# Optimization experiments

Hardware: AMD Instinct MI355X
Metric: run time of the kernel (lower is better)

The kernel has to match this reference:

```python
import jax, jax.numpy as jnp
import numpy as np

B, T, E, V, U = 4096, 80, 100, 10000, 1024


def setup_inputs() -> dict:
    key = jax.random.key(0)
    ks = jax.random.split(key, 8)
    def w(k, shape, fan_in):
        return jax.random.normal(k, shape, jnp.float32) * (1.0 / np.sqrt(fan_in))
    return {
        "inputs": jax.random.randint(ks[0], (B, T), 0, V, dtype=jnp.int32),
        "emb_table": w(ks[1], (V, E), E),
        "Wx0": w(ks[2], (E, U), E),
        "Wh0": w(ks[3], (U, U), U),
        "b0": jnp.zeros((U,), jnp.float32),
        "Wx1": w(ks[4], (U, U), U),
        "Wh1": w(ks[5], (U, U), U),
        "b1": jnp.zeros((U,), jnp.float32),
        "Wfc": w(ks[6], (U, 1), U),
        "bfc": jnp.zeros((1,), jnp.float32),
    }


def reference(inputs, emb_table, Wx0, Wh0, b0, Wx1, Wh1, b1, Wfc, bfc):
    # Embedding lookup: [B, T, E]
    x = emb_table[inputs]
    # Time-major for scan: [T, B, E]
    xs = jnp.swapaxes(x, 0, 1)
    h0_init = jnp.zeros((inputs.shape[0], Wh0.shape[0]), x.dtype)
    h1_init = jnp.zeros((inputs.shape[0], Wh1.shape[0]), x.dtype)

    def step(carry, xt):
        h0, h1 = carry
        # SimpleRNNCell: h' = tanh(x @ Wx + h @ Wh + b); output == new state
        h0 = jnp.tanh(xt @ Wx0 + h0 @ Wh0 + b0)
        h1 = jnp.tanh(h0 @ Wx1 + h1 @ Wh1 + b1)
        return (h0, h1), None

    (h0, h1), _ = jax.lax.scan(step, (h0_init, h1_init), xs)
    # Final dense + sigmoid on last layer-1 output
    prob = jax.nn.sigmoid(h1 @ Wfc + bfc)
    return prob
```

## Files before the change

kernel.cpp:

```cpp
#include <hip/hip_runtime.h>
#include <stdint.h>

#define B_ 4096
#define T_ 80
#define E_ 100
#define V_ 10000
#define U_ 1024

typedef unsigned short u16;
typedef __attribute__((ext_vector_type(8))) __bf16 bf16x8;
typedef __attribute__((ext_vector_type(4))) float f32x4;

__device__ __forceinline__ float bf2f(u16 u) {
    union { unsigned int i; float f; } v; v.i = ((unsigned int)u) << 16; return v.f;
}
__device__ __forceinline__ u16 f2bf(float f) {
    union { float f; unsigned int i; } v; v.f = f;
    unsigned int x = v.i;
    return (u16)((x + 0x7fffu + ((x >> 16) & 1u)) >> 16);
}

__device__ __forceinline__ void load16(const void* g, void* l) {
    __builtin_amdgcn_global_load_lds(
        (__attribute__((address_space(1))) void*)(uintptr_t)g,
        (__attribute__((address_space(3))) void*)(uint32_t)(uintptr_t)l,
        16, 0, 0);
}

__global__ void transpose_pad(const float* __restrict__ src, u16* __restrict__ dst,
                              int K, int N, int Kp)
{
    __shared__ u16 tile[32][33];
    const int k0 = blockIdx.x * 32;
    const int n0 = blockIdx.y * 32;
    const int tx = threadIdx.x & 31;
    const int ty = threadIdx.x >> 5;
#pragma unroll
    for (int i = 0; i < 4; i++) {
        int k = k0 + ty + i * 8;
        tile[ty + i * 8][tx] = (k < K) ? f2bf(src[(size_t)k * N + (n0 + tx)]) : (u16)0;
    }
    __syncthreads();
#pragma unroll
    for (int i = 0; i < 4; i++) {
        int n = n0 + ty + i * 8;
        dst[(size_t)n * Kp + (k0 + tx)] = tile[tx][ty + i * 8];
    }
}

__global__ void embed_pad(const float* __restrict__ emb, u16* __restrict__ dst)
{
    int id = blockIdx.x * 256 + threadIdx.x;
    int v = id >> 7, k = id & 127;
    dst[id] = (k < E_) ? f2bf(emb[v * E_ + k]) : (u16)0;
}

__global__ void __launch_bounds__(256, 2)
rnn_phase(const u16* __restrict__ embP, const int* __restrict__ idx,
          const u16* __restrict__ Wx0T, const u16* __restrict__ Wh0T, const float* __restrict__ b0,
          const u16* __restrict__ Wx1T, const u16* __restrict__ Wh1T, const float* __restrict__ b1,
          const u16* __restrict__ h0r, u16* __restrict__ h0w,
          const u16* __restrict__ h1r, u16* __restrict__ h1w,
          int do0, int do1)
{
    const int linear = blockIdx.x;
    const int layer  = linear & 1;
    if (layer ? !do1 : !do0) return;

    __shared__ u16 As[2][128 * 64];
    __shared__ u16 Bs[2][128 * 64];
    const int tid  = threadIdx.x;
    const int lane = tid & 63;
    const int wave = tid >> 6;
    const int wm = wave >> 1, wn = wave & 1;
    const int sub = linear >> 1;
    const int m0 = (sub & 31) * 128;
    const int n0 = (sub >> 5) * 128;

    const u16 *A1, *W1, *A2, *W2; const float* bias; u16* C; int K1; bool gather;
    if (layer == 0) { A1 = embP; W1 = Wx0T; K1 = 128;  gather = true;  A2 = h0r; W2 = Wh0T; bias = b0; C = h0w; }
    else            { A1 = h0r;  W1 = Wx1T; K1 = 1024; gather = false; A2 = h1r; W2 = Wh1T; bias = b1; C = h1w; }
    const int KB1 = K1 >> 6;
    const int TOT = KB1 + (U_ >> 6);

    const int r8 = lane >> 3;
    const int c8 = lane & 7;

    int gv[4];
    if (gather) {
#pragma unroll
        for (int cc = 0; cc < 4; cc++)
            gv[cc] = idx[(size_t)(m0 + wave * 32 + cc * 8 + r8) * T_];
    }

    const f32x4 z = {0.f, 0.f, 0.f, 0.f};
    f32x4 acc[4][4];
#pragma unroll
    for (int i = 0; i < 4; i++)
#pragma unroll
        for (int j = 0; j < 4; j++) acc[i][j] = z;

    const int l15 = lane & 15, q = lane >> 4, l7 = lane & 7;
    int offA[2][4], offB[2][4];
#pragma unroll
    for (int kk = 0; kk < 2; kk++) {
#pragma unroll
        for (int f = 0; f < 4; f++) {
            const int rA = wm * 64 + f * 16 + l15;
            const int rB = wn * 64 + f * 16 + l15;
            offA[kk][f] = rA * 64 + (((kk * 4 + q) ^ l7) * 8);
            offB[kk][f] = rB * 64 + (((kk * 4 + q) ^ l7) * 8);
        }
    }

    auto stage = [&](int u, int p) {
        u16* Ad = As[p] + wave * 2048;
        u16* Bd = Bs[p] + wave * 2048;
        if (u < KB1) {
            const int k0 = u * 64;
#pragma unroll
            for (int cc = 0; cc < 4; cc++) {
                const int row = wave * 32 + cc * 8 + r8;
                const int scw = (c8 ^ (row & 7)) * 8;
                const u16* ap = gather ? A1 + (size_t)gv[cc] * 128 + k0 + scw
                                       : A1 + (size_t)(m0 + row) * K1 + k0 + scw;
                load16(ap, Ad + cc * 512);
                load16(W1 + (size_t)(n0 + row) * K1 + k0 + scw, Bd + cc * 512);
            }
        } else {
            const int k0 = (u - KB1) * 64;
#pragma unroll
            for (int cc = 0; cc < 4; cc++) {
                const int row = wave * 32 + cc * 8 + r8;
                const int scw = (c8 ^ (row & 7)) * 8;
                load16(A2 + (size_t)(m0 + row) * U_ + k0 + scw, Ad + cc * 512);
                load16(W2 + (size_t)(n0 + row) * U_ + k0 + scw, Bd + cc * 512);
            }
        }
    };

    stage(0, 0);

#pragma unroll 1
    for (int u = 0; u < TOT; ++u) {
        const int p = u & 1;
        __syncthreads();
        if (u + 1 < TOT) stage(u + 1, p ^ 1);
#pragma unroll
        for (int kk = 0; kk < 2; kk++) {
            bf16x8 a[4], b[4];
#pragma unroll
            for (int f = 0; f < 4; f++) {
                a[f] = *reinterpret_cast<const bf16x8*>(As[p] + offA[kk][f]);
                b[f] = *reinterpret_cast<const bf16x8*>(Bs[p] + offB[kk][f]);
            }
#pragma unroll
            for (int i = 0; i < 4; i++)
#pragma unroll
                for (int j = 0; j < 4; j++)
                    acc[i][j] = __builtin_amdgcn_mfma_f32_16x16x32_bf16(a[i], b[j], acc[i][j], 0, 0, 0);
        }
    }

#pragma unroll
    for (int j = 0; j < 4; j++) {
        const int col = n0 + wn * 64 + j * 16 + l15;
        const float bv = bias[col];
#pragma unroll
        for (int i = 0; i < 4; i++) {
#pragma unroll
            for (int r = 0; r < 4; r++) {
                const int row = m0 + wm * 64 + i * 16 + (q << 2) + r;
                float x = acc[i][j][r] + bv;
                x = fminf(15.f, fmaxf(-15.f, x));
                float e = __expf(2.f * x);
                C[(size_t)row * U_ + col] = f2bf((e - 1.f) / (e + 1.f));
            }
        }
    }
}

__global__ void final_dense(const u16* __restrict__ h1, const float* __restrict__ Wfc,
                            const float* __restrict__ bfc, float* __restrict__ out)
{
    const int lane = threadIdx.x & 63;
    const int wave = threadIdx.x >> 6;
    const int row = blockIdx.x * 4 + wave;
    const u16* hp = h1 + (size_t)row * U_ + lane * 16;
    const float* wp = Wfc + lane * 16;
    float s = 0.f;
#pragma unroll
    for (int i = 0; i < 16; i++) s += bf2f(hp[i]) * wp[i];
#pragma unroll
    for (int off = 32; off; off >>= 1) s += __shfl_down(s, off);
    if (lane == 0) {
        float x = s + bfc[0];
        out[row] = 1.f / (1.f + __expf(-x));
    }
}

extern "C" void kernel_launch(void* const* d_in, const int* in_sizes, int n_in,
                              void* d_out, int out_size, void* d_ws, size_t ws_size,
                              hipStream_t stream)
{
    const int*   inputs = (const int*)d_in[0];
    const float* emb    = (const float*)d_in[1];
    const float* Wx0    = (const float*)d_in[2];
    const float* Wh0    = (const float*)d_in[3];
    const float* b0     = (const float*)d_in[4];
    const float* Wx1    = (const float*)d_in[5];
    const float* Wh1    = (const float*)d_in[6];
    const float* b1     = (const float*)d_in[7];
    const float* Wfc    = (const float*)d_in[8];
    const float* bfc    = (const float*)d_in[9];

    char* ws = (char*)d_ws;
    const size_t MB = 1 << 20;
    u16* h0b[2] = { (u16*)(ws + 0 * MB), (u16*)(ws + 8 * MB) };
    u16* h1b[2] = { (u16*)(ws + 16 * MB), (u16*)(ws + 24 * MB) };
    u16* embP = (u16*)(ws + 32 * MB);
    u16* Wx0T = (u16*)(ws + 35 * MB);
    u16* Wh0T = (u16*)(ws + 36 * MB);
    u16* Wx1T = (u16*)(ws + 38 * MB);
    u16* Wh1T = (u16*)(ws + 40 * MB);

    hipMemsetAsync(h0b[1], 0, 8 * MB, stream);
    hipMemsetAsync(h1b[1], 0, 8 * MB, stream);

    embed_pad<<<V_ * 128 / 256, 256, 0, stream>>>(emb, embP);
    transpose_pad<<<dim3(128 / 32, U_ / 32), 256, 0, stream>>>(Wx0, Wx0T, E_, U_, 128);
    transpose_pad<<<dim3(U_ / 32, U_ / 32), 256, 0, stream>>>(Wh0, Wh0T, U_, U_, U_);
    transpose_pad<<<dim3(U_ / 32, U_ / 32), 256, 0, stream>>>(Wx1, Wx1T, U_, U_, U_);
    transpose_pad<<<dim3(U_ / 32, U_ / 32), 256, 0, stream>>>(Wh1, Wh1T, U_, U_, U_);

    for (int p = 0; p <= T_; ++p) {
        const int e = p & 1;
        rnn_phase<<<512, 256, 0, stream>>>(embP, inputs + p,
                                           Wx0T, Wh0T, b0, Wx1T, Wh1T, b1,
                                           h0b[e ^ 1], h0b[e], h1b[e], h1b[e ^ 1],
                                           (int)(p < T_), (int)(p >= 1));
    }
    final_dense<<<B_ / 4, 256, 0, stream>>>(h1b[1], Wfc, bfc, (float*)d_out);
}
```

Baseline: 3.084 ms.

## Widen RNN GEMM tile to 128x256 and halve grid to 256 blocks

Each block now computes a 128x256 output tile with 4x8 MFMA fragments per wave instead of 128x128, which halves the grid to 256 blocks (one per CU on MI355X) and raises arithmetic intensity per loaded A tile. Layer selection moves from the low bit to the high bits of the block index. The larger accumulator and B shared buffer need launch bounds of one block per SM, so there is less latency hiding and register pressure goes up. With 256 blocks the whole machine runs a single wave of work, but a phase where only one layer is active uses just half the CUs.

```diff
diff --git a/kernel.cpp b/kernel.cpp
--- a/kernel.cpp
+++ b/kernel.cpp
@@ -55,7 +55,7 @@
     dst[id] = (k < E_) ? f2bf(emb[v * E_ + k]) : (u16)0;
 }
 
-__global__ void __launch_bounds__(256, 2)
+__global__ void __launch_bounds__(256, 1)
 rnn_phase(const u16* __restrict__ embP, const int* __restrict__ idx,
           const u16* __restrict__ Wx0T, const u16* __restrict__ Wh0T, const float* __restrict__ b0,
           const u16* __restrict__ Wx1T, const u16* __restrict__ Wh1T, const float* __restrict__ b1,
@@ -64,18 +64,18 @@
           int do0, int do1)
 {
     const int linear = blockIdx.x;
-    const int layer  = linear & 1;
+    const int layer  = linear >> 7;
     if (layer ? !do1 : !do0) return;
 
     __shared__ u16 As[2][128 * 64];
-    __shared__ u16 Bs[2][128 * 64];
+    __shared__ u16 Bs[2][256 * 64];
     const int tid  = threadIdx.x;
     const int lane = tid & 63;
     const int wave = tid >> 6;
     const int wm = wave >> 1, wn = wave & 1;
-    const int sub = linear >> 1;
+    const int sub = linear & 127;
     const int m0 = (sub & 31) * 128;
-    const int n0 = (sub >> 5) * 128;
+    const int n0 = (sub >> 5) * 256;
 
     const u16 *A1, *W1, *A2, *W2; const float* bias; u16* C; int K1; bool gather;
     if (layer == 0) { A1 = embP; W1 = Wx0T; K1 = 128;  gather = true;  A2 = h0r; W2 = Wh0T; bias = b0; C = h0w; }
@@ -94,30 +94,35 @@
     }
 
     const f32x4 z = {0.f, 0.f, 0.f, 0.f};
-    f32x4 acc[4][4];
+    f32x4 acc[4][8];
 #pragma unroll
     for (int i = 0; i < 4; i++)
 #pragma unroll
-        for (int j = 0; j < 4; j++) acc[i][j] = z;
+        for (int j = 0; j < 8; j++) acc[i][j] = z;
 
     const int l15 = lane & 15, q = lane >> 4, l7 = lane & 7;
-    int offA[2][4], offB[2][4];
+    int offA[2][4], offB[2][8];
 #pragma unroll
     for (int kk = 0; kk < 2; kk++) {
 #pragma unroll
         for (int f = 0; f < 4; f++) {
             const int rA = wm * 64 + f * 16 + l15;
-            const int rB = wn * 64 + f * 16 + l15;
             offA[kk][f] = rA * 64 + (((kk * 4 + q) ^ l7) * 8);
-            offB[kk][f] = rB * 64 + (((kk * 4 + q) ^ l7) * 8);
+        }
+#pragma unroll
+        for (int g = 0; g < 8; g++) {
+            const int rB = wn * 128 + g * 16 + l15;
+            offB[kk][g] = rB * 64 + (((kk * 4 + q) ^ l7) * 8);
         }
     }
 
     auto stage = [&](int u, int p) {
         u16* Ad = As[p] + wave * 2048;
-        u16* Bd = Bs[p] + wave * 2048;
+        u16* Bd = Bs[p] + wave * 4096;
+        const u16* W    = (u < KB1) ? W1 : W2;
+        const int  kstr = (u < KB1) ? K1 : U_;
+        const int  k0   = (u < KB1) ? u * 64 : (u - KB1) * 64;
         if (u < KB1) {
-            const int k0 = u * 64;
 #pragma unroll
             for (int cc = 0; cc < 4; cc++) {
                 const int row = wave * 32 + cc * 8 + r8;
@@ -125,17 +130,21 @@
                 const u16* ap = gather ? A1 + (size_t)gv[cc] * 128 + k0 + scw
                                        : A1 + (size_t)(m0 + row) * K1 + k0 + scw;
                 load16(ap, Ad + cc * 512);
-                load16(W1 + (size_t)(n0 + row) * K1 + k0 + scw, Bd + cc * 512);
             }
         } else {
-            const int k0 = (u - KB1) * 64;
+            const int k0h = (u - KB1) * 64;
 #pragma unroll
             for (int cc = 0; cc < 4; cc++) {
                 const int row = wave * 32 + cc * 8 + r8;
                 const int scw = (c8 ^ (row & 7)) * 8;
-                load16(A2 + (size_t)(m0 + row) * U_ + k0 + scw, Ad + cc * 512);
-                load16(W2 + (size_t)(n0 + row) * U_ + k0 + scw, Bd + cc * 512);
+                load16(A2 + (size_t)(m0 + row) * U_ + k0h + scw, Ad + cc * 512);
             }
+        }
+#pragma unroll
+        for (int cc = 0; cc < 8; cc++) {
+            const int row = wave * 64 + cc * 8 + r8;
+            const int scw = (c8 ^ (row & 7)) * 8;
+            load16(W + (size_t)(n0 + row) * kstr + k0 + scw, Bd + cc * 512);
         }
     };
 
@@ -148,23 +157,24 @@
         if (u + 1 < TOT) stage(u + 1, p ^ 1);
 #pragma unroll
         for (int kk = 0; kk < 2; kk++) {
-            bf16x8 a[4], b[4];
-#pragma unroll
-            for (int f = 0; f < 4; f++) {
+            bf16x8 a[4], b[8];
+#pragma unroll
+            for (int f = 0; f < 4; f++)
                 a[f] = *reinterpret_cast<const bf16x8*>(As[p] + offA[kk][f]);
-                b[f] = *reinterpret_cast<const bf16x8*>(Bs[p] + offB[kk][f]);
-            }
+#pragma unroll
+            for (int g = 0; g < 8; g++)
+                b[g] = *reinterpret_cast<const bf16x8*>(Bs[p] + offB[kk][g]);
 #pragma unroll
             for (int i = 0; i < 4; i++)
 #pragma unroll
-                for (int j = 0; j < 4; j++)
+                for (int j = 0; j < 8; j++)
                     acc[i][j] = __builtin_amdgcn_mfma_f32_16x16x32_bf16(a[i], b[j], acc[i][j], 0, 0, 0);
         }
     }
 
 #pragma unroll
-    for (int j = 0; j < 4; j++) {
-        const int col = n0 + wn * 64 + j * 16 + l15;
+    for (int j = 0; j < 8; j++) {
+        const int col = n0 + wn * 128 + j * 16 + l15;
         const float bv = bias[col];
 #pragma unroll
         for (int i = 0; i < 4; i++) {
@@ -235,7 +245,7 @@
 
     for (int p = 0; p <= T_; ++p) {
         const int e = p & 1;
-        rnn_phase<<<512, 256, 0, stream>>>(embP, inputs + p,
+        rnn_phase<<<256, 256, 0, stream>>>(embP, inputs + p,
                                            Wx0T, Wh0T, b0, Wx1T, Wh1T, b1,
                                            h0b[e ^ 1], h0b[e], h1b[e], h1b[e ^ 1],
                                            (int)(p < T_), (int)(p >= 1));
```

New measurement: 3.371 ms. +9.3%, slower.
